# Performance work log

Measured on AMD Instinct MI355X. Metric: run time of the kernel, lower is better.

## Reference

```python
import jax, jax.numpy as jnp
import numpy as np

EPS = 1e-12  # matches torch F.normalize default eps
TARGET_N = 6.0  # target_compression_N


def _l2_normalize(v):
    n = jnp.linalg.norm(v, axis=-1, keepdims=True)
    return v / jnp.maximum(n, EPS)


def setup_inputs() -> dict:
    key = jax.random.key(0)
    k1, k2, k3 = jax.random.split(key, 3)
    B, L, D = 4, 8192, 1024
    x = jax.random.normal(k1, (B, L, D), dtype=jnp.float32)
    # nn.Linear weights (out, in), applied as x @ W.T
    Wq = jax.random.normal(k2, (D, D), dtype=jnp.float32) * (1.0 / np.sqrt(D))
    Wk = jax.random.normal(k3, (D, D), dtype=jnp.float32) * (1.0 / np.sqrt(D))
    return {"x": x, "Wq": Wq, "Wk": Wk}


def reference(x, Wq, Wk):
    B, L, D = x.shape
    q = jnp.einsum('bld,ed->ble', x, Wq)
    k = jnp.einsum('bld,ed->ble', x, Wk)
    q_norm = _l2_normalize(q)
    k_norm = _l2_normalize(k)
    k_prev = jnp.roll(k_norm, shift=1, axis=1)
    cos_sim = jnp.sum(q_norm * k_prev, axis=-1)          # (B, L)
    p = 0.5 * (1.0 - cos_sim)
    p = p.at[:, 0].set(1.0)
    b = (p >= 0.5).astype(x.dtype)
    b = b.at[:, 0].set(1.0)

    F_val = jnp.mean(b)
    G_val = jnp.mean(p)
    N = TARGET_N
    ratio_loss = N / (N - 1.0) * ((N - 1.0) * F_val * G_val + (1.0 - F_val) * (1.0 - G_val))

    # Stream compaction via cumsum-based scatter.  Lc_max is data dependent in
    # the torch code; for jit-compatibility we pad the compressed axis to L.
    mask = b > 0.5                                        # (B, L) bool
    dest = jnp.cumsum(b.astype(jnp.int32), axis=1) - 1   # destination slot per boundary
    dest = jnp.clip(dest, 0, L - 1)
    bidx = jnp.broadcast_to(jnp.arange(B, dtype=jnp.int32)[:, None], (B, L))
    # Non-boundary positions contribute exact zeros (x * mask), so colliding
    # destinations from clipped/non-boundary entries are harmless under add.
    x_down = jnp.zeros((B, L, D), dtype=x.dtype).at[bidx, dest].add(x * mask[..., None])
    P_down = jnp.zeros((B, L), dtype=p.dtype).at[bidx, dest].add(p * mask)
    lengths = jnp.sum(b, axis=1).astype(jnp.int32)        # (B,)

    return x_down, P_down, b, p, lengths, ratio_loss
```

## Files before the change

### kernel.cpp

```cpp
#include <hip/hip_runtime.h>
#include <stdint.h>
#include <stddef.h>

typedef __attribute__((ext_vector_type(8)))  _Float16 f16x8;
typedef __attribute__((ext_vector_type(16))) float    f32x16;
typedef __attribute__((ext_vector_type(4)))  float    f32x4;
typedef __attribute__((ext_vector_type(4)))  unsigned int u32x4;

#define B_ 4
#define L_ 8192
#define D_ 1024
#define BL 32768
#define XROWS 32769
#define XCV_BYTES (256u * XROWS * 16u)
#define WCV_BYTES (256u * 1024u * 16u)
#define BUFSZ 65792u

__device__ __forceinline__ void gload16(const void* g, void* l){
  __builtin_amdgcn_global_load_lds((const __attribute__((address_space(1))) void*)g,
                                   (__attribute__((address_space(3))) void*)l, 16, 0, 0);
}

__global__ void k0_cvt(const float* __restrict__ x, const float* __restrict__ Wq,
                       const float* __restrict__ Wk, unsigned char* __restrict__ xcv)
{
  __shared__ unsigned short hi[64][128];
  __shared__ unsigned short lo[64][128];
  const int bx = blockIdx.x, kt = blockIdx.y, tid = threadIdx.x;
  const float* src; unsigned char* dst; int rowstride, pad, rt;
  if (bx < 512){ src = x;  dst = xcv;                         rowstride = XROWS; pad = 1; rt = bx; }
  else if (bx < 528){ src = Wq; dst = xcv + XCV_BYTES;        rowstride = 1024;  pad = 0; rt = bx - 512; }
  else { src = Wk; dst = xcv + XCV_BYTES + WCV_BYTES;         rowstride = 1024;  pad = 0; rt = bx - 528; }

  #pragma unroll
  for (int it = 0; it < 8; ++it){
    int idx = it*256 + tid;
    int r = idx >> 5, q4 = idx & 31;
    f32x4 v = *(const f32x4*)(src + (size_t)(rt*64 + r)*1024 + kt*128 + q4*4);
    #pragma unroll
    for (int j = 0; j < 4; ++j){
      float f = v[j];
      _Float16 h = (_Float16)f;
      _Float16 l = (_Float16)(f - (float)h);
      hi[r][q4*4+j] = __builtin_bit_cast(unsigned short, h);
      lo[r][q4*4+j] = __builtin_bit_cast(unsigned short, l);
    }
  }
  __syncthreads();
  #pragma unroll
  for (int it = 0; it < 8; ++it){
    int seg = it*4 + (tid>>6);
    int r = tid & 63;
    int ksl = seg >> 3, c = seg & 7;
    const unsigned short* plane = (c < 4) ? &hi[0][0] : &lo[0][0];
    int kl = ksl*32 + (c & 3)*8;
    u32x4 val = *(const u32x4*)(plane + r*128 + kl);
    int ksg = kt*4 + ksl;
    size_t off = (((size_t)(ksg*8 + c)) * rowstride + (pad + rt*64 + r)) * 16;
    *(u32x4*)(dst + off) = val;
  }
}

__launch_bounds__(512, 2)
__global__ void k1_f16(const unsigned char* __restrict__ xcv,
                       float* __restrict__ dotS, float* __restrict__ nqS,
                       float* __restrict__ nkS)
{
  __shared__ __align__(16) unsigned char lds[2 * BUFSZ];
  const int tid = threadIdx.x, lane = tid & 63, w = tid >> 6;
  const int wr = w >> 1, wc = w & 1;
  const int bid = blockIdx.x;
  const int strip = (bid & 7) + ((bid >> 6) << 3);
  const int echunk = (bid >> 3) & 7;
  const int row0 = strip << 8;
  const int col0 = echunk << 7;
  const int l31 = lane & 31, lh = lane >> 5;

  unsigned goff[9], stride[9]; int loff[9];
  #pragma unroll
  for (int j = 0; j < 9; ++j){
    int cj = w*9 + j;
    if (cj < 40){
      int c = cj / 5, s = cj - c*5;
      int rr0  = (s < 4) ? s*64   : 193;
      int subo = (s < 4) ? s*1024 : 3088;
      goff[j] = ((unsigned)c*XROWS + (unsigned)(row0 + rr0))*16u + (unsigned)lane*16u;
      loff[j] = c*4128 + subo;
      stride[j] = 8u*XROWS*16u;
    } else if (cj < 56){
      int idx = cj - 40, c = idx >> 1, h = idx & 1;
      goff[j] = XCV_BYTES + ((unsigned)c*1024u + (unsigned)(col0 + h*64))*16u + (unsigned)lane*16u;
      loff[j] = 33024 + c*2048 + h*1024;
      stride[j] = 131072u;
    } else {
      int idx = cj - 56, c = idx >> 1, h = idx & 1;
      goff[j] = XCV_BYTES + WCV_BYTES + ((unsigned)c*1024u + (unsigned)(col0 + h*64))*16u + (unsigned)lane*16u;
      loff[j] = 33024 + 16384 + c*2048 + h*1024;
      stride[j] = 131072u;
    }
  }

  const unsigned bq  = (unsigned)(wr*64 + l31 + 1)*16u + (unsigned)lh*4128u;
  const unsigned bk  = bq - 16u;
  const unsigned bwq = 33024u + (unsigned)(wc*64 + l31)*16u + (unsigned)lh*2048u;
  const unsigned bwk = bwq + 16384u;

  f32x16 accq[2][2] = {}, acck[2][2] = {};

  #pragma unroll
  for (int j = 0; j < 9; ++j){ gload16(xcv + goff[j], lds + loff[j]); goff[j] += stride[j]; }
  __syncthreads();

  for (int ks = 0; ks < 32; ++ks){
    const unsigned cur = (ks & 1) ? BUFSZ : 0u;
    const unsigned nxt = cur ^ BUFSZ;
    if (ks < 31){
      #pragma unroll
      for (int j = 0; j < 9; ++j){ gload16(xcv + goff[j], lds + loff[j] + nxt); goff[j] += stride[j]; }
    }
    #pragma unroll
    for (int kk = 0; kk < 2; ++kk){
      f16x8 aq[2][2], ak[2][2];
      #pragma unroll
      for (int mt = 0; mt < 2; ++mt)
        #pragma unroll
        for (int hl = 0; hl < 2; ++hl){
          unsigned ao = cur + mt*512u + kk*8256u + hl*16512u;
          aq[mt][hl] = *(const f16x8*)(lds + bq + ao);
          ak[mt][hl] = *(const f16x8*)(lds + bk + ao);
        }
      __builtin_amdgcn_s_setprio(1);
      #pragma unroll
      for (int n = 0; n < 2; ++n){
        unsigned boq = cur + bwq + n*512u + kk*4096u;
        unsigned bok = cur + bwk + n*512u + kk*4096u;
        f16x8 bqh = *(const f16x8*)(lds + boq);
        f16x8 bql = *(const f16x8*)(lds + boq + 8192u);
        f16x8 bkh = *(const f16x8*)(lds + bok);
        f16x8 bkl = *(const f16x8*)(lds + bok + 8192u);
        #pragma unroll
        for (int mt = 0; mt < 2; ++mt){
          accq[mt][n] = __builtin_amdgcn_mfma_f32_32x32x16_f16(aq[mt][0], bqh, accq[mt][n], 0, 0, 0);
          accq[mt][n] = __builtin_amdgcn_mfma_f32_32x32x16_f16(aq[mt][0], bql, accq[mt][n], 0, 0, 0);
          accq[mt][n] = __builtin_amdgcn_mfma_f32_32x32x16_f16(aq[mt][1], bqh, accq[mt][n], 0, 0, 0);
          acck[mt][n] = __builtin_amdgcn_mfma_f32_32x32x16_f16(ak[mt][0], bkh, acck[mt][n], 0, 0, 0);
          acck[mt][n] = __builtin_amdgcn_mfma_f32_32x32x16_f16(ak[mt][0], bkl, acck[mt][n], 0, 0, 0);
          acck[mt][n] = __builtin_amdgcn_mfma_f32_32x32x16_f16(ak[mt][1], bkh, acck[mt][n], 0, 0, 0);
        }
      }
      __builtin_amdgcn_s_setprio(0);
    }
    __syncthreads();
  }

  f32x16 dvv[2], qvv[2], kvv[2];
  #pragma unroll
  for (int mt = 0; mt < 2; ++mt){
    dvv[mt] = accq[mt][0]*acck[mt][0] + accq[mt][1]*acck[mt][1];
    qvv[mt] = accq[mt][0]*accq[mt][0] + accq[mt][1]*accq[mt][1];
    kvv[mt] = acck[mt][0]*acck[mt][0] + acck[mt][1]*acck[mt][1];
  }
  #pragma unroll
  for (int m = 1; m < 32; m <<= 1){
    #pragma unroll
    for (int mt = 0; mt < 2; ++mt)
      #pragma unroll
      for (int r = 0; r < 16; ++r){
        dvv[mt][r] += __shfl_xor(dvv[mt][r], m, 64);
        qvv[mt][r] += __shfl_xor(qvv[mt][r], m, 64);
        kvv[mt][r] += __shfl_xor(kvv[mt][r], m, 64);
      }
  }
  float* scr = (float*)lds;
  if (l31 == 0 && wc == 1){
    #pragma unroll
    for (int mt = 0; mt < 2; ++mt)
      #pragma unroll
      for (int r = 0; r < 16; ++r){
        int rm = (r & 3) + ((r >> 2) << 3) + (lh << 2);
        int ti = (wr*2 + mt)*32 + rm;
        scr[ti] = dvv[mt][r]; scr[256 + ti] = qvv[mt][r]; scr[512 + ti] = kvv[mt][r];
      }
  }
  __syncthreads();
  if (l31 == 0 && wc == 0){
    #pragma unroll
    for (int mt = 0; mt < 2; ++mt)
      #pragma unroll
      for (int r = 0; r < 16; ++r){
        int rm = (r & 3) + ((r >> 2) << 3) + (lh << 2);
        int ti = (wr*2 + mt)*32 + rm;
        int grow = row0 + wr*64 + mt*32 + rm;
        size_t idx = (size_t)echunk * BL + grow;
        dotS[idx] = dvv[mt][r] + scr[ti];
        nqS[idx]  = qvv[mt][r] + scr[256 + ti];
        nkS[idx]  = kvv[mt][r] + scr[512 + ti];
      }
  }
}

__global__ void k2_scan(const float* __restrict__ dotS, const float* __restrict__ nqS,
                        const float* __restrict__ nkS,
                        float* __restrict__ p_out, float* __restrict__ b_out,
                        float* __restrict__ len_out, int* __restrict__ invmap,
                        float* __restrict__ bat_sums, int* __restrict__ lenI, int nparts)
{
  const int batch = blockIdx.x;
  const int tid   = threadIdx.x;
  const int lane  = tid & 63, wv = tid >> 6;
  const int lbase = tid << 3;
  float ps = 0.f; int bc = 0; unsigned bits = 0;
  #pragma unroll
  for (int j = 0; j < 8; ++j){
    const int l = lbase + j;
    const int g = batch * L_ + l;
    float dt = 0.f, nq = 0.f, nk = 0.f;
    for (int e = 0; e < nparts; ++e){
      dt += dotS[(size_t)e*BL + g]; nq += nqS[(size_t)e*BL + g]; nk += nkS[(size_t)e*BL + g];
    }
    float p;
    if (l == 0) p = 1.f;
    else {
      const float dn = fmaxf(sqrtf(nq), 1e-12f) * fmaxf(sqrtf(nk), 1e-12f);
      p = 0.5f * (1.f - dt / dn);
    }
    const int bb = (p >= 0.5f) ? 1 : 0;
    p_out[g] = p;
    b_out[g] = (float)bb;
    ps += p; bc += bb; bits |= (unsigned)bb << j;
  }
  int sc = bc;
  #pragma unroll
  for (int m = 1; m < 64; m <<= 1){
    int t = __shfl_up(sc, m, 64);
    if (lane >= m) sc += t;
  }
  float pss = ps;
  #pragma unroll
  for (int m = 1; m < 64; m <<= 1) pss += __shfl_xor(pss, m, 64);

  __shared__ int wsum[16];
  __shared__ float wps[16];
  if (lane == 63) wsum[wv] = sc;
  if (lane == 0)  wps[wv] = pss;
  __syncthreads();
  if (tid < 16){
    int v = wsum[tid];
    #pragma unroll
    for (int m = 1; m < 16; m <<= 1){
      int t = __shfl_up(v, m, 64);
      if (tid >= m) v += t;
    }
    wsum[tid] = v;
  }
  __syncthreads();
  const int waveoff = (wv == 0) ? 0 : wsum[wv - 1];
  const int total = wsum[15];
  int run = waveoff + sc - bc;
  #pragma unroll
  for (int j = 0; j < 8; ++j){
    if ((bits >> j) & 1u){ invmap[batch * L_ + run] = lbase + j; ++run; }
  }
  if (tid == 0){
    float psum = 0.f;
    #pragma unroll
    for (int i = 0; i < 16; ++i) psum += wps[i];
    bat_sums[batch]     = (float)total;
    bat_sums[4 + batch] = psum;
    lenI[batch]    = total;
    len_out[batch] = (float)total;
  }
}

__global__ void k3_fill(const float* __restrict__ x, const float* __restrict__ p_out,
                        const int* __restrict__ invmap, const int* __restrict__ lenI,
                        const float* __restrict__ bat_sums,
                        float* __restrict__ xdown, float* __restrict__ Pdown,
                        float* __restrict__ loss_out)
{
  const int bid = blockIdx.x, tid = threadIdx.x;
  #pragma unroll 4
  for (int i = 0; i < 16; ++i){
    const int s = bid*16 + i;
    const int batch = s >> 13, j = s & 8191;
    const int len = lenI[batch];
    const int inb = (j < len) ? 1 : 0;
    const int src = inb ? invmap[batch * L_ + j] : 0;
    f32x4 v = {0.f, 0.f, 0.f, 0.f};
    if (inb) v = *(const f32x4*)(x + (((size_t)(batch * L_ + src)) << 10) + (tid << 2));
    *(f32x4*)(xdown + (((size_t)(batch * L_ + j)) << 10) + (tid << 2)) = v;
    if (tid == 0) Pdown[batch * L_ + j] = inb ? p_out[batch * L_ + src] : 0.f;
  }
  if (bid == 0 && tid == 0){
    const float F = (bat_sums[0] + bat_sums[1] + bat_sums[2] + bat_sums[3]) * (1.f / 32768.f);
    const float G = (bat_sums[4] + bat_sums[5] + bat_sums[6] + bat_sums[7]) * (1.f / 32768.f);
    loss_out[0] = 1.2f * (5.f * F * G + (1.f - F) * (1.f - G));
  }
}

extern "C" void kernel_launch(void* const* d_in, const int* in_sizes, int n_in,
                              void* d_out, int out_size, void* d_ws, size_t ws_size,
                              hipStream_t stream)
{
  const float* x  = (const float*)d_in[0];
  const float* Wq = (const float*)d_in[1];
  const float* Wk = (const float*)d_in[2];

  float* out      = (float*)d_out;
  float* xdown    = out;
  float* Pdown    = out + (size_t)BL * D_;
  float* b_out    = Pdown + BL;
  float* p_out    = b_out + BL;
  float* len_out  = p_out + BL;
  float* loss_out = len_out + B_;

  unsigned char* xcv = (unsigned char*)d_ws;
  float* dotS     = (float*)(xcv + XCV_BYTES + 2*WCV_BYTES);
  float* nqS      = dotS + (size_t)8*BL;
  float* nkS      = nqS + (size_t)8*BL;
  int*   invmap   = (int*)(nkS + (size_t)8*BL);
  float* bat_sums = (float*)(invmap + BL);
  int*   lenI     = (int*)(bat_sums + 8);

  hipLaunchKernelGGL(k0_cvt, dim3(544, 8), dim3(256), 0, stream, x, Wq, Wk, xcv);
  hipLaunchKernelGGL(k1_f16, dim3(1024), dim3(512), 0, stream, xcv, dotS, nqS, nkS);
  hipLaunchKernelGGL(k2_scan, dim3(4), dim3(1024), 0, stream,
                     dotS, nqS, nkS, p_out, b_out, len_out, invmap, bat_sums, lenI, 8);
  hipLaunchKernelGGL(k3_fill, dim3(2048), dim3(256), 0, stream,
                     x, p_out, invmap, lenI, bat_sums, xdown, Pdown, loss_out);
}
```

Before: 745.2 us.

## Use 4-stage LDS pipeline, swizzled layout, drop overlap row, stitch strip boundaries

```diff
diff --git a/kernel.cpp b/kernel.cpp
--- a/kernel.cpp
+++ b/kernel.cpp
@@ -11,154 +11,180 @@
 #define L_ 8192
 #define D_ 1024
 #define BL 32768
-#define XROWS 32769
-#define XCV_BYTES (256u * XROWS * 16u)
+#define XR 32768
+#define XCV_BYTES (256u * XR * 16u)
 #define WCV_BYTES (256u * 1024u * 16u)
-#define BUFSZ 65792u
 
 __device__ __forceinline__ void gload16(const void* g, void* l){
   __builtin_amdgcn_global_load_lds((const __attribute__((address_space(1))) void*)g,
                                    (__attribute__((address_space(3))) void*)l, 16, 0, 0);
 }
 
+__device__ __forceinline__ f32x16 MF(f16x8 a, f16x8 b, f32x16 c){
+  return __builtin_amdgcn_mfma_f32_32x32x16_f16(a, b, c, 0, 0, 0);
+}
+
 __global__ void k0_cvt(const float* __restrict__ x, const float* __restrict__ Wq,
                        const float* __restrict__ Wk, unsigned char* __restrict__ xcv)
 {
   __shared__ unsigned short hi[64][128];
   __shared__ unsigned short lo[64][128];
   const int bx = blockIdx.x, kt = blockIdx.y, tid = threadIdx.x;
-  const float* src; unsigned char* dst; int rowstride, pad, rt;
-  if (bx < 512){ src = x;  dst = xcv;                         rowstride = XROWS; pad = 1; rt = bx; }
-  else if (bx < 528){ src = Wq; dst = xcv + XCV_BYTES;        rowstride = 1024;  pad = 0; rt = bx - 512; }
-  else { src = Wk; dst = xcv + XCV_BYTES + WCV_BYTES;         rowstride = 1024;  pad = 0; rt = bx - 528; }
+  const float* src; unsigned char* dst; int rs, rt;
+  if (bx < 512){ src = x;  dst = xcv;                         rs = XR;   rt = bx; }
+  else if (bx < 528){ src = Wq; dst = xcv + XCV_BYTES;        rs = 1024; rt = bx - 512; }
+  else { src = Wk; dst = xcv + XCV_BYTES + WCV_BYTES;         rs = 1024; rt = bx - 528; }
 
   #pragma unroll
   for (int it = 0; it < 8; ++it){
     int idx = it*256 + tid;
     int r = idx >> 5, q4 = idx & 31;
     f32x4 v = *(const f32x4*)(src + (size_t)(rt*64 + r)*1024 + kt*128 + q4*4);
+    int swb = ((q4 >> 1) ^ (r & 15))*8 + (q4 & 1)*4;
     #pragma unroll
     for (int j = 0; j < 4; ++j){
       float f = v[j];
       _Float16 h = (_Float16)f;
       _Float16 l = (_Float16)(f - (float)h);
-      hi[r][q4*4+j] = __builtin_bit_cast(unsigned short, h);
-      lo[r][q4*4+j] = __builtin_bit_cast(unsigned short, l);
+      hi[r][swb + j] = __builtin_bit_cast(unsigned short, h);
+      lo[r][swb + j] = __builtin_bit_cast(unsigned short, l);
     }
   }
   __syncthreads();
   #pragma unroll
   for (int it = 0; it < 8; ++it){
-    int seg = it*4 + (tid>>6);
+    int seg = it*4 + (tid >> 6);
     int r = tid & 63;
     int ksl = seg >> 3, c = seg & 7;
     const unsigned short* plane = (c < 4) ? &hi[0][0] : &lo[0][0];
     int kl = ksl*32 + (c & 3)*8;
-    u32x4 val = *(const u32x4*)(plane + r*128 + kl);
-    int ksg = kt*4 + ksl;
-    size_t off = (((size_t)(ksg*8 + c)) * rowstride + (pad + rt*64 + r)) * 16;
-    *(u32x4*)(dst + off) = val;
+    u32x4 val = *(const u32x4*)(plane + r*128 + ((((kl >> 3) ^ (r & 15))) << 3));
+    int P = (kt*4 + ksl)*8 + c;
+    *(u32x4*)(dst + ((size_t)P * rs + rt*64 + r) * 16) = val;
   }
 }
 
 __launch_bounds__(512, 2)
 __global__ void k1_f16(const unsigned char* __restrict__ xcv,
-                       float* __restrict__ dotS, float* __restrict__ nqS,
-                       float* __restrict__ nkS)
-{
-  __shared__ __align__(16) unsigned char lds[2 * BUFSZ];
+                       float* __restrict__ dotP, float* __restrict__ nqP,
+                       float* __restrict__ nkP,
+                       float* __restrict__ qface, float* __restrict__ kface)
+{
+  __shared__ __align__(16) unsigned char lds[131072];
   const int tid = threadIdx.x, lane = tid & 63, w = tid >> 6;
-  const int wr = w >> 1, wc = w & 1;
+  const int wr = w >> 1, wc = w & 1, l31 = lane & 31, lh = lane >> 5;
   const int bid = blockIdx.x;
   const int strip = (bid & 7) + ((bid >> 6) << 3);
-  const int echunk = (bid >> 3) & 7;
-  const int row0 = strip << 8;
-  const int col0 = echunk << 7;
-  const int l31 = lane & 31, lh = lane >> 5;
-
-  unsigned goff[9], stride[9]; int loff[9];
-  #pragma unroll
-  for (int j = 0; j < 9; ++j){
-    int cj = w*9 + j;
-    if (cj < 40){
-      int c = cj / 5, s = cj - c*5;
-      int rr0  = (s < 4) ? s*64   : 193;
-      int subo = (s < 4) ? s*1024 : 3088;
-      goff[j] = ((unsigned)c*XROWS + (unsigned)(row0 + rr0))*16u + (unsigned)lane*16u;
-      loff[j] = c*4128 + subo;
-      stride[j] = 8u*XROWS*16u;
-    } else if (cj < 56){
-      int idx = cj - 40, c = idx >> 1, h = idx & 1;
-      goff[j] = XCV_BYTES + ((unsigned)c*1024u + (unsigned)(col0 + h*64))*16u + (unsigned)lane*16u;
-      loff[j] = 33024 + c*2048 + h*1024;
-      stride[j] = 131072u;
+  const int ec = (bid >> 3) & 7;
+  const int row0 = strip << 8, col0 = ec << 7;
+
+  unsigned goff[4]; int loff[4]; unsigned d0[4], d1[4];
+  #pragma unroll
+  for (int j = 0; j < 4; ++j){
+    int cj = w*4 + j;
+    if (cj < 16){
+      int lp = cj >> 2, sub = cj & 3;
+      int cg = (lp & 1) + ((lp >> 1) << 2);
+      goff[j] = ((unsigned)cg * XR + (unsigned)(row0 + sub*64 + lane)) * 16u;
+      loff[j] = lp*4096 + (sub*64 + lane)*16;
+      d0[j] = 2u*XR*16u; d1[j] = 6u*XR*16u;
+    } else if (cj < 24){
+      int t = cj - 16, lp = t >> 1, hf = t & 1;
+      int cg = (lp & 1) + ((lp >> 1) << 2);
+      goff[j] = XCV_BYTES + ((unsigned)cg * 1024u + (unsigned)(col0 + hf*64 + lane)) * 16u;
+      loff[j] = 16384 + lp*2048 + (hf*64 + lane)*16;
+      d0[j] = 32768u; d1[j] = 98304u;
     } else {
-      int idx = cj - 56, c = idx >> 1, h = idx & 1;
-      goff[j] = XCV_BYTES + WCV_BYTES + ((unsigned)c*1024u + (unsigned)(col0 + h*64))*16u + (unsigned)lane*16u;
-      loff[j] = 33024 + 16384 + c*2048 + h*1024;
-      stride[j] = 131072u;
-    }
-  }
-
-  const unsigned bq  = (unsigned)(wr*64 + l31 + 1)*16u + (unsigned)lh*4128u;
-  const unsigned bk  = bq - 16u;
-  const unsigned bwq = 33024u + (unsigned)(wc*64 + l31)*16u + (unsigned)lh*2048u;
-  const unsigned bwk = bwq + 16384u;
+      int t = cj - 24, lp = t >> 1, hf = t & 1;
+      int cg = (lp & 1) + ((lp >> 1) << 2);
+      goff[j] = XCV_BYTES + WCV_BYTES + ((unsigned)cg * 1024u + (unsigned)(col0 + hf*64 + lane)) * 16u;
+      loff[j] = 24576 + lp*2048 + (hf*64 + lane)*16;
+      d0[j] = 32768u; d1[j] = 98304u;
+    }
+  }
+
+  #define STAGE(slot) { _Pragma("unroll") \
+    for (int j = 0; j < 4; ++j) gload16(xcv + goff[j], lds + (slot) + loff[j]); }
+  #define ADV(par) { _Pragma("unroll") \
+    for (int j = 0; j < 4; ++j) goff[j] += (par) ? d1[j] : d0[j]; }
+
+  STAGE(0u)      ADV(0)
+  STAGE(32768u)  ADV(1)
+  STAGE(65536u)  ADV(0)
+
+  const unsigned ab = (unsigned)(lh*4096) + (unsigned)((wr*64 + l31)*16);
+  const unsigned bb = 16384u + (unsigned)(lh*2048) + (unsigned)((wc*64 + l31)*16);
 
   f32x16 accq[2][2] = {}, acck[2][2] = {};
 
-  #pragma unroll
-  for (int j = 0; j < 9; ++j){ gload16(xcv + goff[j], lds + loff[j]); goff[j] += stride[j]; }
-  __syncthreads();
-
-  for (int ks = 0; ks < 32; ++ks){
-    const unsigned cur = (ks & 1) ? BUFSZ : 0u;
-    const unsigned nxt = cur ^ BUFSZ;
-    if (ks < 31){
-      #pragma unroll
-      for (int j = 0; j < 9; ++j){ gload16(xcv + goff[j], lds + loff[j] + nxt); goff[j] += stride[j]; }
-    }
-    #pragma unroll
-    for (int kk = 0; kk < 2; ++kk){
-      f16x8 aq[2][2], ak[2][2];
-      #pragma unroll
-      for (int mt = 0; mt < 2; ++mt)
-        #pragma unroll
-        for (int hl = 0; hl < 2; ++hl){
-          unsigned ao = cur + mt*512u + kk*8256u + hl*16512u;
-          aq[mt][hl] = *(const f16x8*)(lds + bq + ao);
-          ak[mt][hl] = *(const f16x8*)(lds + bk + ao);
-        }
+  for (int h = 0; h < 64; ++h){
+    if (h < 62)      { asm volatile("s_waitcnt vmcnt(8)" ::: "memory"); }
+    else if (h == 62){ asm volatile("s_waitcnt vmcnt(4)" ::: "memory"); }
+    else             { asm volatile("s_waitcnt vmcnt(0)" ::: "memory"); }
+    __builtin_amdgcn_s_barrier();
+    if (h < 61){ unsigned s3 = (unsigned)((h+3) & 3) * 32768u; STAGE(s3) ADV((h+3) & 1) }
+    const unsigned cur = (unsigned)(h & 3) * 32768u;
+    f16x8 ah[2], al[2];
+    ah[0] = *(const f16x8*)(lds + cur + ab);
+    ah[1] = *(const f16x8*)(lds + cur + ab + 512u);
+    al[0] = *(const f16x8*)(lds + cur + ab + 8192u);
+    al[1] = *(const f16x8*)(lds + cur + ab + 8704u);
+    #pragma unroll
+    for (int n = 0; n < 2; ++n){
+      unsigned bo = cur + bb + (unsigned)n*512u;
+      f16x8 qh = *(const f16x8*)(lds + bo);
+      f16x8 ql = *(const f16x8*)(lds + bo + 4096u);
+      f16x8 kh = *(const f16x8*)(lds + bo + 8192u);
+      f16x8 kl_ = *(const f16x8*)(lds + bo + 12288u);
       __builtin_amdgcn_s_setprio(1);
       #pragma unroll
-      for (int n = 0; n < 2; ++n){
-        unsigned boq = cur + bwq + n*512u + kk*4096u;
-        unsigned bok = cur + bwk + n*512u + kk*4096u;
-        f16x8 bqh = *(const f16x8*)(lds + boq);
-        f16x8 bql = *(const f16x8*)(lds + boq + 8192u);
-        f16x8 bkh = *(const f16x8*)(lds + bok);
-        f16x8 bkl = *(const f16x8*)(lds + bok + 8192u);
-        #pragma unroll
-        for (int mt = 0; mt < 2; ++mt){
-          accq[mt][n] = __builtin_amdgcn_mfma_f32_32x32x16_f16(aq[mt][0], bqh, accq[mt][n], 0, 0, 0);
-          accq[mt][n] = __builtin_amdgcn_mfma_f32_32x32x16_f16(aq[mt][0], bql, accq[mt][n], 0, 0, 0);
-          accq[mt][n] = __builtin_amdgcn_mfma_f32_32x32x16_f16(aq[mt][1], bqh, accq[mt][n], 0, 0, 0);
-          acck[mt][n] = __builtin_amdgcn_mfma_f32_32x32x16_f16(ak[mt][0], bkh, acck[mt][n], 0, 0, 0);
-          acck[mt][n] = __builtin_amdgcn_mfma_f32_32x32x16_f16(ak[mt][0], bkl, acck[mt][n], 0, 0, 0);
-          acck[mt][n] = __builtin_amdgcn_mfma_f32_32x32x16_f16(ak[mt][1], bkh, acck[mt][n], 0, 0, 0);
-        }
+      for (int mt = 0; mt < 2; ++mt){
+        accq[mt][n] = MF(ah[mt], qh, accq[mt][n]);
+        accq[mt][n] = MF(ah[mt], ql, accq[mt][n]);
+        accq[mt][n] = MF(al[mt], qh, accq[mt][n]);
+        acck[mt][n] = MF(ah[mt], kh, acck[mt][n]);
+        acck[mt][n] = MF(ah[mt], kl_, acck[mt][n]);
+        acck[mt][n] = MF(al[mt], kh, acck[mt][n]);
       }
       __builtin_amdgcn_s_setprio(0);
     }
-    __syncthreads();
-  }
-
+  }
+
+  __syncthreads();
+  float* kbuf = (float*)lds;
+  #pragma unroll
+  for (int mt = 0; mt < 2; ++mt)
+    #pragma unroll
+    for (int r = 0; r < 16; ++r){
+      int rm = (r & 3) + ((r >> 2) << 3) + (lh << 2);
+      int rl = wr*64 + mt*32 + rm;
+      kbuf[rl*128 + wc*64 + l31]      = acck[mt][0][r];
+      kbuf[rl*128 + wc*64 + 32 + l31] = acck[mt][1][r];
+    }
+  __syncthreads();
   f32x16 dvv[2], qvv[2], kvv[2];
   #pragma unroll
   for (int mt = 0; mt < 2; ++mt){
-    dvv[mt] = accq[mt][0]*acck[mt][0] + accq[mt][1]*acck[mt][1];
     qvv[mt] = accq[mt][0]*accq[mt][0] + accq[mt][1]*accq[mt][1];
     kvv[mt] = acck[mt][0]*acck[mt][0] + acck[mt][1]*acck[mt][1];
+    #pragma unroll
+    for (int r = 0; r < 16; ++r){
+      int rm = (r & 3) + ((r >> 2) << 3) + (lh << 2);
+      int rl = wr*64 + mt*32 + rm;
+      int cl = rl - 1; if (cl < 0) cl = 0;
+      float k0v = kbuf[cl*128 + wc*64 + l31];
+      float k1v = kbuf[cl*128 + wc*64 + 32 + l31];
+      dvv[mt][r] = accq[mt][0][r]*k0v + accq[mt][1][r]*k1v;
+    }
+  }
+  __syncthreads();
+  if (wr == 0 && lh == 0){
+    qface[strip*1024 + ec*128 + wc*64 + l31]      = accq[0][0][0];
+    qface[strip*1024 + ec*128 + wc*64 + 32 + l31] = accq[0][1][0];
+  }
+  if (wr == 3 && lh == 1){
+    kface[strip*1024 + ec*128 + wc*64 + l31]      = acck[1][0][15];
+    kface[strip*1024 + ec*128 + wc*64 + 32 + l31] = acck[1][1][15];
   }
   #pragma unroll
   for (int m = 1; m < 32; m <<= 1){
@@ -190,39 +216,65 @@
       for (int r = 0; r < 16; ++r){
         int rm = (r & 3) + ((r >> 2) << 3) + (lh << 2);
         int ti = (wr*2 + mt)*32 + rm;
-        int grow = row0 + wr*64 + mt*32 + rm;
-        size_t idx = (size_t)echunk * BL + grow;
-        dotS[idx] = dvv[mt][r] + scr[ti];
-        nqS[idx]  = qvv[mt][r] + scr[256 + ti];
-        nkS[idx]  = kvv[mt][r] + scr[512 + ti];
-      }
-  }
-}
-
-__global__ void k2_scan(const float* __restrict__ dotS, const float* __restrict__ nqS,
-                        const float* __restrict__ nkS,
+        size_t idx = (size_t)ec * BL + row0 + wr*64 + mt*32 + rm;
+        dotP[idx] = dvv[mt][r] + scr[ti];
+        nqP[idx]  = qvv[mt][r] + scr[256 + ti];
+        nkP[idx]  = kvv[mt][r] + scr[512 + ti];
+      }
+  }
+}
+
+__global__ void k15_reduce(float* __restrict__ dotP, float* __restrict__ nqP,
+                           float* __restrict__ nkP)
+{
+  int idx = blockIdx.x*1024 + threadIdx.x;
+  float* base = (idx < 32768) ? dotP : (idx < 65536 ? nqP : nkP);
+  int row = idx & 32767;
+  float s = 0.f;
+  #pragma unroll
+  for (int e = 0; e < 8; ++e) s += base[(size_t)e*BL + row];
+  base[row] = s;
+}
+
+__global__ void k2_scan(const float* __restrict__ dotF, const float* __restrict__ nqF,
+                        const float* __restrict__ nkF,
+                        const float* __restrict__ qface, const float* __restrict__ kface,
                         float* __restrict__ p_out, float* __restrict__ b_out,
                         float* __restrict__ len_out, int* __restrict__ invmap,
-                        float* __restrict__ bat_sums, int* __restrict__ lenI, int nparts)
+                        float* __restrict__ bat_sums, int* __restrict__ lenI)
 {
   const int batch = blockIdx.x;
   const int tid   = threadIdx.x;
   const int lane  = tid & 63, wv = tid >> 6;
-  const int lbase = tid << 3;
+  const int lb    = tid << 3;
+  const int g0    = batch * L_ + lb;
+
+  float dta[8], nqa[8], nka[8];
+  *(f32x4*)(dta)   = *(const f32x4*)(dotF + g0); *(f32x4*)(dta+4) = *(const f32x4*)(dotF + g0 + 4);
+  *(f32x4*)(nqa)   = *(const f32x4*)(nqF + g0);  *(f32x4*)(nqa+4) = *(const f32x4*)(nqF + g0 + 4);
+  *(f32x4*)(nka)   = *(const f32x4*)(nkF + g0);  *(f32x4*)(nka+4) = *(const f32x4*)(nkF + g0 + 4);
+  float nkp = (lb > 0) ? nkF[g0 - 1] : 0.f;
+
   float ps = 0.f; int bc = 0; unsigned bits = 0;
   #pragma unroll
   for (int j = 0; j < 8; ++j){
-    const int l = lbase + j;
+    const int l = lb + j;
     const int g = batch * L_ + l;
-    float dt = 0.f, nq = 0.f, nk = 0.f;
-    for (int e = 0; e < nparts; ++e){
-      dt += dotS[(size_t)e*BL + g]; nq += nqS[(size_t)e*BL + g]; nk += nkS[(size_t)e*BL + g];
-    }
     float p;
     if (l == 0) p = 1.f;
     else {
-      const float dn = fmaxf(sqrtf(nq), 1e-12f) * fmaxf(sqrtf(nk), 1e-12f);
-      p = 0.5f * (1.f - dt / dn);
+      float dt = dta[j];
+      if ((l & 255) == 0){
+        int s = g >> 8;
+        const f32x4* qf = (const f32x4*)(qface + (size_t)s*1024);
+        const f32x4* kf = (const f32x4*)(kface + (size_t)(s-1)*1024);
+        f32x4 a4 = {0.f,0.f,0.f,0.f};
+        for (int i = 0; i < 256; ++i) a4 += qf[i]*kf[i];
+        dt = a4[0] + a4[1] + a4[2] + a4[3];
+      }
+      float nkprev = j ? nka[j-1] : nkp;
+      float dn = fmaxf(sqrtf(nqa[j]), 1e-12f) * fmaxf(sqrtf(nkprev), 1e-12f);
+      p = 0.5f * (1.f - dt/dn);
     }
     const int bb = (p >= 0.5f) ? 1 : 0;
     p_out[g] = p;
@@ -259,7 +311,7 @@
   int run = waveoff + sc - bc;
   #pragma unroll
   for (int j = 0; j < 8; ++j){
-    if ((bits >> j) & 1u){ invmap[batch * L_ + run] = lbase + j; ++run; }
+    if ((bits >> j) & 1u){ invmap[batch * L_ + run] = lb + j; ++run; }
   }
   if (tid == 0){
     float psum = 0.f;
@@ -314,18 +366,24 @@
   float* len_out  = p_out + BL;
   float* loss_out = len_out + B_;
 
+  float* qface = xdown + (size_t)4*1024*1024;
+  float* kface = qface + 131072;
+
   unsigned char* xcv = (unsigned char*)d_ws;
-  float* dotS     = (float*)(xcv + XCV_BYTES + 2*WCV_BYTES);
-  float* nqS      = dotS + (size_t)8*BL;
-  float* nkS      = nqS + (size_t)8*BL;
-  int*   invmap   = (int*)(nkS + (size_t)8*BL);
+  float* dotP     = (float*)(xcv + XCV_BYTES + 2*WCV_BYTES);
+  float* nqP      = dotP + (size_t)8*BL;
+  float* nkP      = nqP + (size_t)8*BL;
+  int*   invmap   = (int*)(nkP + (size_t)8*BL);
   float* bat_sums = (float*)(invmap + BL);
   int*   lenI     = (int*)(bat_sums + 8);
 
   hipLaunchKernelGGL(k0_cvt, dim3(544, 8), dim3(256), 0, stream, x, Wq, Wk, xcv);
-  hipLaunchKernelGGL(k1_f16, dim3(1024), dim3(512), 0, stream, xcv, dotS, nqS, nkS);
+  hipLaunchKernelGGL(k1_f16, dim3(1024), dim3(512), 0, stream,
+                     xcv, dotP, nqP, nkP, qface, kface);
+  hipLaunchKernelGGL(k15_reduce, dim3(96), dim3(1024), 0, stream, dotP, nqP, nkP);
   hipLaunchKernelGGL(k2_scan, dim3(4), dim3(1024), 0, stream,
-                     dotS, nqS, nkS, p_out, b_out, len_out, invmap, bat_sums, lenI, 8);
+                     dotP, nqP, nkP, qface, kface,
+                     p_out, b_out, len_out, invmap, bat_sums, lenI);
   hipLaunchKernelGGL(k3_fill, dim3(2048), dim3(256), 0, stream,
                      x, p_out, invmap, lenI, bat_sums, xdown, Pdown, loss_out);
 }
```

Result: faster. 716.1 us (-3.9%).
